# Kernel optimization log

Hardware: AMD Instinct MI355X
Metric: run time of the kernel (lower is better)

## Reference

```python
import jax, jax.numpy as jnp
import numpy as np

B, I_LEN, Q_LEN, H = 256, 256, 64, 512
MID, G, FLAT_OUT = 512, 1, 1024


def setup_inputs() -> dict:
    key = jax.random.key(0)
    ks = jax.random.split(key, 20)
    s = lambda k, sh: jax.random.normal(k, sh, dtype=jnp.float32) * 0.02
    inp = {
        'i_batch': jax.random.normal(ks[0], (B, I_LEN, H), dtype=jnp.float32),
        'q_batch': jax.random.normal(ks[1], (B, Q_LEN, H), dtype=jnp.float32),
        'i_mask': jax.random.bernoulli(ks[2], 0.1, (B, 1, 1, I_LEN)),
        'q_mask': jax.random.bernoulli(ks[3], 0.1, (B, 1, 1, Q_LEN)),
        # l_flatten (applied to i_feat) params
        'lf_w1': s(ks[4], (H, MID)), 'lf_b1': jnp.zeros((MID,), jnp.float32),
        'lf_w2': s(ks[5], (MID, G)), 'lf_b2': jnp.zeros((G,), jnp.float32),
        'lf_wm': s(ks[6], (H * G, FLAT_OUT)), 'lf_bm': jnp.zeros((FLAT_OUT,), jnp.float32),
        # i_flatten (applied to l_feat) params
        'if_w1': s(ks[7], (H, MID)), 'if_b1': jnp.zeros((MID,), jnp.float32),
        'if_w2': s(ks[8], (MID, G)), 'if_b2': jnp.zeros((G,), jnp.float32),
        'if_wm': s(ks[9], (H * G, FLAT_OUT)), 'if_bm': jnp.zeros((FLAT_OUT,), jnp.float32),
        # fh_h: Linear(1024, 512)
        'fh_w': s(ks[10], (FLAT_OUT, 512)), 'fh_b': jnp.zeros((512,), jnp.float32),
    }
    return inp


def _qkv_attention(query, key, value, mask):
    # query [B,Lq,H], key/value [B,Lk,H], mask [B,1,1,Lk] (True = pad)
    d_k = query.shape[-1]
    scores = jnp.einsum('bqh,bkh->bqk', query, key) / jnp.sqrt(jnp.asarray(d_k, query.dtype))
    scores = jnp.where(mask[:, 0], jnp.asarray(-65504.0, scores.dtype), scores)
    p_attn = jax.nn.softmax(scores, axis=-1)
    return jnp.einsum('bqk,bkh->bqh', p_attn, value)


def _att_flat(x, x_mask, w1, b1, w2, b2, wm, bm):
    # x [B,L,H], x_mask [B,1,1,L]
    att = jnp.maximum(x @ w1 + b1, 0.0) @ w2 + b2           # [B,L,G]
    att = jnp.where(x_mask[:, 0, 0, :, None], -1e9, att)
    att = jax.nn.softmax(att, axis=1)
    pooled = jnp.einsum('blg,blh->bgh', att, x).reshape(x.shape[0], -1)  # [B,G*H]
    return pooled @ wm + bm, att[..., 0]                    # att.squeeze() with G=1


def reference(i_batch, q_batch, i_mask, q_mask,
              lf_w1, lf_b1, lf_w2, lf_b2, lf_wm, lf_bm,
              if_w1, if_b1, if_w2, if_b2, if_wm, if_bm,
              fh_w, fh_b):
    i_feat = _qkv_attention(i_batch, q_batch, q_batch, q_mask)   # [B,I_LEN,H]
    i_feat, i_weight = _att_flat(i_feat, i_mask, lf_w1, lf_b1, lf_w2, lf_b2, lf_wm, lf_bm)
    l_feat = _qkv_attention(q_batch, i_batch, i_batch, i_mask)   # [B,Q_LEN,H]
    l_feat, _ = _att_flat(l_feat, q_mask, if_w1, if_b1, if_w2, if_b2, if_wm, if_bm)
    out = (l_feat + i_feat) @ fh_w + fh_b                        # [B,512]
    return out, i_weight
```

## Files before the change

kernel.cpp:

```cpp
#include <hip/hip_runtime.h>
#include <math.h>


#define SCALE 0.04419417382415922f

typedef __attribute__((ext_vector_type(8))) short short8;
typedef __attribute__((ext_vector_type(4))) float floatx4;

__device__ __forceinline__ unsigned short f2bf(float x) {
  unsigned u = __float_as_uint(x);
  unsigned r = u + 0x7FFFu + ((u >> 16) & 1u);
  return (unsigned short)(r >> 16);
}
__device__ __forceinline__ float bf2f(unsigned short h) {
  return __uint_as_float(((unsigned)h) << 16);
}
__device__ __forceinline__ unsigned pk2(float a, float b) {
  return (unsigned)f2bf(a) | ((unsigned)f2bf(b) << 16);
}

__device__ __forceinline__ float wave_max(float v) {
#pragma unroll
  for (int o = 32; o > 0; o >>= 1) v = fmaxf(v, __shfl_xor(v, o, 64));
  return v;
}
__device__ __forceinline__ float wave_sum(float v) {
#pragma unroll
  for (int o = 32; o > 0; o >>= 1) v += __shfl_xor(v, o, 64);
  return v;
}

#define GLD_LDS16(gptr, lptr)                                             \
  __builtin_amdgcn_global_load_lds(                                       \
      (const __attribute__((address_space(1))) void*)(gptr),              \
      (__attribute__((address_space(3))) void*)(lptr), 16, 0, 0)

__global__ __launch_bounds__(256) void k_prep(
    const float* __restrict__ ib, const float* __restrict__ qb,
    const float* __restrict__ lf_w1, const float* __restrict__ if_w1,
    const float* __restrict__ lf_wm, const float* __restrict__ if_wm,
    const float* __restrict__ fh_w, unsigned short* __restrict__ ib_bf,
    unsigned short* __restrict__ ibT, unsigned short* __restrict__ qb_bf,
    unsigned short* __restrict__ w1t_lf, unsigned short* __restrict__ w1t_if,
    unsigned short* __restrict__ wcat_t, unsigned short* __restrict__ fh_wt) {
  __shared__ __align__(16) char smem[64 * 65 * 4];
  const int idx = blockIdx.x, t = threadIdx.x;

  if (idx < 512) {
    float(*T)[65] = (float(*)[65])smem;
    const float* src;
    unsigned short* dst;
    int N, ds, koff, k0, n0;
    if (idx < 64) {
      src = lf_w1; dst = w1t_lf; N = 512; ds = 512; koff = 0;
      k0 = (idx & 7) * 64; n0 = (idx >> 3) * 64;
    } else if (idx < 128) {
      int l = idx - 64;
      src = if_w1; dst = w1t_if; N = 512; ds = 512; koff = 0;
      k0 = (l & 7) * 64; n0 = (l >> 3) * 64;
    } else if (idx < 256) {
      int l = idx - 128;
      src = lf_wm; dst = wcat_t; N = 1024; ds = 1024; koff = 0;
      k0 = (l & 7) * 64; n0 = (l >> 3) * 64;
    } else if (idx < 384) {
      int l = idx - 256;
      src = if_wm; dst = wcat_t; N = 1024; ds = 1024; koff = 512;
      k0 = (l & 7) * 64; n0 = (l >> 3) * 64;
    } else {
      int l = idx - 384;
      src = fh_w; dst = fh_wt; N = 512; ds = 1024; koff = 0;
      k0 = (l & 15) * 64; n0 = (l >> 4) * 64;
    }
#pragma unroll
    for (int i = 0; i < 16; i++) {
      int e = t + i * 256, r = e >> 6, c = e & 63;
      T[r][c] = src[(size_t)(k0 + r) * N + n0 + c];
    }
    __syncthreads();
#pragma unroll
    for (int i = 0; i < 8; i++) {
      int e = t + i * 256, r = e >> 5, c2 = (e & 31) * 2;
      *(unsigned*)&dst[(size_t)(n0 + r) * ds + koff + k0 + c2] =
          pk2(T[c2][r], T[c2 + 1][r]);
    }
  } else if (idx < 4608) {
    int j = idx - 512;
    int b = j >> 4, tok0 = ((j >> 2) & 3) * 64, h0 = (j & 3) * 128;
    unsigned short* Tb = (unsigned short*)smem;
    const float* src = ib + ((size_t)b * 256 + tok0) * 512 + h0;
#pragma unroll
    for (int i = 0; i < 8; i++) {
      int e = t + i * 256, tok = e >> 5, h4 = (e & 31) * 4;
      float4 v = *(const float4*)&src[(size_t)tok * 512 + h4];
      uint2 p;
      p.x = pk2(v.x, v.y);
      p.y = pk2(v.z, v.w);
      int col = ((((h4 >> 3) ^ (tok >> 3)) & 15) << 3) | (h4 & 7);
      *(uint2*)&Tb[tok * 128 + col] = p;
    }
    __syncthreads();
    unsigned short* dbf = ib_bf + ((size_t)b * 256 + tok0) * 512 + h0;
#pragma unroll
    for (int i = 0; i < 4; i++) {
      int e = t + i * 256, tok = e >> 4, g = e & 15;
      int sg = (g ^ (tok >> 3)) & 15;
      *(uint4*)&dbf[(size_t)tok * 512 + g * 8] = *(const uint4*)&Tb[tok * 128 + sg * 8];
    }
    unsigned short* dT = ibT + ((size_t)b * 512 + h0) * 256 + tok0;
#pragma unroll
    for (int i = 0; i < 4; i++) {
      int e = t + i * 256, h = e >> 3, tc = (e & 7) * 8;
      int hg = h >> 3, ho = h & 7;
      unsigned y[8];
#pragma unroll
      for (int k = 0; k < 8; k++) {
        int r = tc + k;
        y[k] = Tb[r * 128 + (((hg ^ (r >> 3)) & 15) << 3) + ho];
      }
      uint4 v;
      v.x = y[0] | (y[1] << 16);
      v.y = y[2] | (y[3] << 16);
      v.z = y[4] | (y[5] << 16);
      v.w = y[6] | (y[7] << 16);
      *(uint4*)&dT[(size_t)h * 256 + tc] = v;
    }
  } else {
    int j = idx - 4608;
    const float4* src = (const float4*)(qb + (size_t)j * 4096);
    uint2* dst = (uint2*)(qb_bf + (size_t)j * 4096);
#pragma unroll
    for (int i = 0; i < 4; i++) {
      int e = t + i * 256;
      float4 v = src[e];
      uint2 p;
      p.x = pk2(v.x, v.y);
      p.y = pk2(v.z, v.w);
      dst[e] = p;
    }
  }
}

__global__ __launch_bounds__(256) void k_scores_f(
    const unsigned short* __restrict__ ibf, const unsigned short* __restrict__ qbf,
    const int* __restrict__ imask, const int* __restrict__ qmask,
    unsigned short* __restrict__ P1, unsigned short* __restrict__ P2,
    float* __restrict__ psum) {
  __shared__ unsigned short As[64 * 64];
  __shared__ unsigned short Bs[128 * 64];
  __shared__ __align__(16) unsigned short X[128 * 72];
  const int b = blockIdx.y, ic = blockIdx.x, i0 = ic * 128;
  const int t = threadIdx.x, w = t >> 6, lane = t & 63, c = lane & 15, qq = lane >> 4;

  floatx4 acc[4][2];
#pragma unroll
  for (int ti = 0; ti < 4; ti++)
#pragma unroll
    for (int tj = 0; tj < 2; tj++) acc[ti][tj] = (floatx4){0.f, 0.f, 0.f, 0.f};

  for (int k0 = 0; k0 < 512; k0 += 64) {
#pragma unroll
    for (int i = 0; i < 2; i++) {
      int s = i * 256 + t, row = s >> 3, src = (s & 7) ^ (row & 7);
      GLD_LDS16(qbf + ((size_t)b * 64 + row) * 512 + k0 + src * 8,
                &As[(i * 256 + w * 64) * 8]);
    }
#pragma unroll
    for (int i = 0; i < 4; i++) {
      int s = i * 256 + t, row = s >> 3, src = (s & 7) ^ (row & 7);
      GLD_LDS16(ibf + ((size_t)b * 256 + i0 + row) * 512 + k0 + src * 8,
                &Bs[(i * 256 + w * 64) * 8]);
    }
    __syncthreads();
#pragma unroll
    for (int kk = 0; kk < 2; kk++) {
      short8 a[4], bb[2];
#pragma unroll
      for (int ti = 0; ti < 4; ti++)
        a[ti] = *(const short8*)&As[(ti * 16 + c) * 64 + ((kk * 4 + qq) ^ (c & 7)) * 8];
#pragma unroll
      for (int tj = 0; tj < 2; tj++)
        bb[tj] = *(const short8*)&Bs[(w * 32 + tj * 16 + c) * 64 + ((kk * 4 + qq) ^ (c & 7)) * 8];
#pragma unroll
      for (int ti = 0; ti < 4; ti++)
#pragma unroll
        for (int tj = 0; tj < 2; tj++)
          acc[ti][tj] = __builtin_amdgcn_mfma_f32_16x16x32_bf16(a[ti], bb[tj], acc[ti][tj], 0, 0, 0);
    }
    __syncthreads();
  }

  const int il0 = w * 32 + c;
  int imsk0 = imask[b * 256 + i0 + il0];
  int imsk1 = imask[b * 256 + i0 + il0 + 16];
  int qm[4][4];
#pragma unroll
  for (int ti = 0; ti < 4; ti++)
#pragma unroll
    for (int rr = 0; rr < 4; rr++) qm[ti][rr] = qmask[b * 64 + ti * 16 + qq * 4 + rr];

#pragma unroll
  for (int ti = 0; ti < 4; ti++)
#pragma unroll
    for (int rr = 0; rr < 4; rr++) {
      int qv = ti * 16 + qq * 4 + rr;
      float e0 = imsk0 ? 0.f : __expf(acc[ti][0][rr] * SCALE);
      float e1 = imsk1 ? 0.f : __expf(acc[ti][1][rr] * SCALE);
      X[qv * 136 + il0] = f2bf(e0);
      X[qv * 136 + il0 + 16] = f2bf(e1);
      float s = e0 + e1;
#pragma unroll
      for (int o = 1; o <= 8; o <<= 1) s += __shfl_xor(s, o, 64);
      if (c == 0) psum[((size_t)(b * 64 + qv)) * 8 + ic * 4 + w] = s;
    }
  __syncthreads();
#pragma unroll
  for (int i = 0; i < 4; i++) {
    int e2 = t + i * 256, qv = e2 >> 4, g = e2 & 15;
    *(uint4*)&P2[((size_t)b * 64 + qv) * 256 + i0 + g * 8] = *(const uint4*)&X[qv * 136 + g * 8];
  }
  __syncthreads();

#pragma unroll
  for (int tj = 0; tj < 2; tj++) {
    float ev[4][4];
    float s1 = 0.f;
#pragma unroll
    for (int ti = 0; ti < 4; ti++)
#pragma unroll
      for (int rr = 0; rr < 4; rr++) {
        ev[ti][rr] = qm[ti][rr] ? 0.f : __expf(acc[ti][tj][rr] * SCALE);
        s1 += ev[ti][rr];
      }
    s1 += __shfl_xor(s1, 16, 64);
    s1 += __shfl_xor(s1, 32, 64);
    float inv = 1.f / s1;
    int il = il0 + tj * 16;
#pragma unroll
    for (int ti = 0; ti < 4; ti++)
#pragma unroll
      for (int rr = 0; rr < 4; rr++)
        X[il * 72 + ti * 16 + qq * 4 + rr] = f2bf(ev[ti][rr] * inv);
  }
  __syncthreads();
#pragma unroll
  for (int i = 0; i < 4; i++) {
    int e2 = t + i * 256, il = e2 >> 3, g = e2 & 7;
    *(uint4*)&P1[((size_t)b * 256 + i0 + il) * 64 + g * 8] = *(const uint4*)&X[il * 72 + g * 8];
  }
}

__global__ __launch_bounds__(256) void k_av2(const unsigned short* __restrict__ P2,
                                             const unsigned short* __restrict__ ibT,
                                             const float* __restrict__ psum,
                                             unsigned short* __restrict__ lfeat) {
  __shared__ unsigned short As[64 * 64];
  __shared__ unsigned short Bs[128 * 64];
  const int b = blockIdx.y, n0 = blockIdx.x * 128;
  const int t = threadIdx.x, w = t >> 6, lane = t & 63, c = lane & 15, q = lane >> 4;
  const int wm = w >> 1, wn = w & 1;
  floatx4 acc[2][4];
#pragma unroll
  for (int ti = 0; ti < 2; ti++)
#pragma unroll
    for (int tj = 0; tj < 4; tj++) acc[ti][tj] = (floatx4){0.f, 0.f, 0.f, 0.f};

  for (int kc = 0; kc < 256; kc += 64) {
#pragma unroll
    for (int i = 0; i < 2; i++) {
      int s = i * 256 + t, row = s >> 3, src = (s & 7) ^ (row & 7);
      GLD_LDS16(P2 + ((size_t)b * 64 + row) * 256 + kc + src * 8, &As[(i * 256 + w * 64) * 8]);
    }
#pragma unroll
    for (int i = 0; i < 4; i++) {
      int s = i * 256 + t, row = s >> 3, src = (s & 7) ^ (row & 7);
      GLD_LDS16(ibT + ((size_t)b * 512 + n0 + row) * 256 + kc + src * 8,
                &Bs[(i * 256 + w * 64) * 8]);
    }
    __syncthreads();
#pragma unroll
    for (int kk = 0; kk < 2; kk++) {
      short8 a[2], bb[4];
#pragma unroll
      for (int ti = 0; ti < 2; ti++)
        a[ti] = *(const short8*)&As[(wm * 32 + ti * 16 + c) * 64 + ((kk * 4 + q) ^ (c & 7)) * 8];
#pragma unroll
      for (int tj = 0; tj < 4; tj++)
        bb[tj] = *(const short8*)&Bs[(wn * 64 + tj * 16 + c) * 64 + ((kk * 4 + q) ^ (c & 7)) * 8];
#pragma unroll
      for (int ti = 0; ti < 2; ti++)
#pragma unroll
        for (int tj = 0; tj < 4; tj++)
          acc[ti][tj] = __builtin_amdgcn_mfma_f32_16x16x32_bf16(a[ti], bb[tj], acc[ti][tj], 0, 0, 0);
    }
    __syncthreads();
  }
#pragma unroll
  for (int ti = 0; ti < 2; ti++)
#pragma unroll
    for (int rr = 0; rr < 4; rr++) {
      int m = wm * 32 + ti * 16 + q * 4 + rr;
      const float* ps = psum + ((size_t)(b * 64 + m)) * 8;
      float s = ps[0] + ps[1] + ps[2] + ps[3] + ps[4] + ps[5] + ps[6] + ps[7];
      float inv = 1.f / s;
      unsigned short* op = lfeat + ((size_t)b * 64 + m) * 512 + n0 + wn * 64;
#pragma unroll
      for (int tj = 0; tj < 4; tj++) op[tj * 16 + c] = f2bf(acc[ti][tj][rr] * inv);
    }
}

__global__ __launch_bounds__(256) void k_qbw1(const unsigned short* __restrict__ qbf,
                                              const unsigned short* __restrict__ W1t,
                                              unsigned short* __restrict__ qbW1T) {
  __shared__ unsigned short As[64 * 64];
  __shared__ unsigned short Bs[128 * 64];
  const int b = blockIdx.y, n0 = blockIdx.x * 128;
  const int t = threadIdx.x, w = t >> 6, lane = t & 63, c = lane & 15, q = lane >> 4;
  const int wm = w >> 1, wn = w & 1;
  floatx4 acc[2][4];
#pragma unroll
  for (int ti = 0; ti < 2; ti++)
#pragma unroll
    for (int tj = 0; tj < 4; tj++) acc[ti][tj] = (floatx4){0.f, 0.f, 0.f, 0.f};

  for (int k0 = 0; k0 < 512; k0 += 64) {
#pragma unroll
    for (int i = 0; i < 2; i++) {
      int s = i * 256 + t, row = s >> 3, src = (s & 7) ^ (row & 7);
      GLD_LDS16(qbf + ((size_t)b * 64 + row) * 512 + k0 + src * 8,
                &As[(i * 256 + w * 64) * 8]);
    }
#pragma unroll
    for (int i = 0; i < 4; i++) {
      int s = i * 256 + t, row = s >> 3, src = (s & 7) ^ (row & 7);
      GLD_LDS16(W1t + (size_t)(n0 + row) * 512 + k0 + src * 8,
                &Bs[(i * 256 + w * 64) * 8]);
    }
    __syncthreads();
#pragma unroll
    for (int kk = 0; kk < 2; kk++) {
      short8 a[2], bb[4];
#pragma unroll
      for (int ti = 0; ti < 2; ti++)
        a[ti] = *(const short8*)&As[(wm * 32 + ti * 16 + c) * 64 + ((kk * 4 + q) ^ (c & 7)) * 8];
#pragma unroll
      for (int tj = 0; tj < 4; tj++)
        bb[tj] = *(const short8*)&Bs[(wn * 64 + tj * 16 + c) * 64 + ((kk * 4 + q) ^ (c & 7)) * 8];
#pragma unroll
      for (int ti = 0; ti < 2; ti++)
#pragma unroll
        for (int tj = 0; tj < 4; tj++)
          acc[ti][tj] = __builtin_amdgcn_mfma_f32_16x16x32_bf16(a[ti], bb[tj], acc[ti][tj], 0, 0, 0);
    }
    __syncthreads();
  }
#pragma unroll
  for (int ti = 0; ti < 2; ti++)
#pragma unroll
    for (int tj = 0; tj < 4; tj++) {
      int n = n0 + wn * 64 + tj * 16 + c;
      int m = wm * 32 + ti * 16 + q * 4;
      uint2 p;
      p.x = pk2(acc[ti][tj][0], acc[ti][tj][1]);
      p.y = pk2(acc[ti][tj][2], acc[ti][tj][3]);
      *(uint2*)&qbW1T[((size_t)b * 512 + n) * 64 + m] = p;
    }
}

__global__ __launch_bounds__(256) void k_logits_i64(
    const unsigned short* __restrict__ P1, const unsigned short* __restrict__ qbW1T,
    const float* __restrict__ b1, const float* __restrict__ w2,
    float* __restrict__ outp) {
  __shared__ unsigned short As[128 * 64];
  __shared__ unsigned short Bs[128 * 64];
  __shared__ float red[2][128];
  const int b = blockIdx.y;
  const int mt = blockIdx.x & 1, nc = blockIdx.x >> 1;
  const int m0 = mt * 128, n0 = nc * 128;
  const int t = threadIdx.x, w = t >> 6, lane = t & 63, c = lane & 15, q = lane >> 4;
  const int wm = w >> 1, wn = w & 1;

#pragma unroll
  for (int i = 0; i < 4; i++) {
    int s = i * 256 + t, row = s >> 3, src = (s & 7) ^ (row & 7);
    GLD_LDS16(P1 + ((size_t)b * 256 + m0 + row) * 64 + src * 8, &As[(i * 256 + w * 64) * 8]);
  }
#pragma unroll
  for (int i = 0; i < 4; i++) {
    int s = i * 256 + t, row = s >> 3, src = (s & 7) ^ (row & 7);
    GLD_LDS16(qbW1T + ((size_t)b * 512 + n0 + row) * 64 + src * 8, &Bs[(i * 256 + w * 64) * 8]);
  }
  __syncthreads();
  floatx4 acc[4][4];
#pragma unroll
  for (int ti = 0; ti < 4; ti++)
#pragma unroll
    for (int tj = 0; tj < 4; tj++) acc[ti][tj] = (floatx4){0.f, 0.f, 0.f, 0.f};
#pragma unroll
  for (int kk = 0; kk < 2; kk++) {
    short8 a[4], bb[4];
#pragma unroll
    for (int ti = 0; ti < 4; ti++)
      a[ti] = *(const short8*)&As[(wm * 64 + ti * 16 + c) * 64 + ((kk * 4 + q) ^ (c & 7)) * 8];
#pragma unroll
    for (int tj = 0; tj < 4; tj++)
      bb[tj] = *(const short8*)&Bs[(wn * 64 + tj * 16 + c) * 64 + ((kk * 4 + q) ^ (c & 7)) * 8];
#pragma unroll
    for (int ti = 0; ti < 4; ti++)
#pragma unroll
      for (int tj = 0; tj < 4; tj++)
        acc[ti][tj] = __builtin_amdgcn_mfma_f32_16x16x32_bf16(a[ti], bb[tj], acc[ti][tj], 0, 0, 0);
  }

  float partial[4][4] = {};
#pragma unroll
  for (int tj = 0; tj < 4; tj++) {
    int n = n0 + wn * 64 + tj * 16 + c;
    float bia = b1[n], wwv = w2[n];
#pragma unroll
    for (int ti = 0; ti < 4; ti++)
#pragma unroll
      for (int r = 0; r < 4; r++)
        partial[ti][r] += fmaxf(acc[ti][tj][r] + bia, 0.f) * wwv;
  }
#pragma unroll
  for (int msk = 1; msk <= 8; msk <<= 1)
#pragma unroll
    for (int ti = 0; ti < 4; ti++)
#pragma unroll
      for (int r = 0; r < 4; r++)
        partial[ti][r] += __shfl_xor(partial[ti][r], msk, 64);
  if (c == 0) {
#pragma unroll
    for (int ti = 0; ti < 4; ti++)
#pragma unroll
      for (int r = 0; r < 4; r++)
        red[wn][wm * 64 + ti * 16 + q * 4 + r] = partial[ti][r];
  }
  __syncthreads();
  if (t < 128) outp[(size_t)nc * 65536 + b * 256 + m0 + t] = red[0][t] + red[1][t];
}

__global__ __launch_bounds__(256) void k_logits_part(
    const unsigned short* __restrict__ X, const unsigned short* __restrict__ W1t,
    const float* __restrict__ b1, const float* __restrict__ w2,
    float* __restrict__ outp, int M) {
  __shared__ unsigned short As[128 * 64];
  __shared__ unsigned short Bs[128 * 64];
  __shared__ float red[2][128];
  const int t = threadIdx.x, w = t >> 6, lane = t & 63;
  const int wm = w >> 1, wn = w & 1, c = lane & 15, q = lane >> 4;
  const int idx = blockIdx.x;
  const int m_tile = (idx & 7) + ((idx >> 5) << 3), nc = (idx >> 3) & 3;
  const int m0 = m_tile * 128, n0 = nc * 128;

  floatx4 acc[4][4];
#pragma unroll
  for (int ti = 0; ti < 4; ti++)
#pragma unroll
    for (int tj = 0; tj < 4; tj++) acc[ti][tj] = (floatx4){0.f, 0.f, 0.f, 0.f};

  for (int k0 = 0; k0 < 512; k0 += 64) {
#pragma unroll
    for (int it = 0; it < 4; it++) {
      int s = it * 256 + t, row = s >> 3, src = (s & 7) ^ (row & 7);
      GLD_LDS16(X + (size_t)(m0 + row) * 512 + k0 + src * 8, &As[(it * 256 + w * 64) * 8]);
      GLD_LDS16(W1t + (size_t)(n0 + row) * 512 + k0 + src * 8, &Bs[(it * 256 + w * 64) * 8]);
    }
    __syncthreads();
#pragma unroll
    for (int kk = 0; kk < 2; kk++) {
      short8 a[4], bb[4];
#pragma unroll
      for (int ti = 0; ti < 4; ti++)
        a[ti] = *(const short8*)&As[(wm * 64 + ti * 16 + c) * 64 + ((kk * 4 + q) ^ (c & 7)) * 8];
#pragma unroll
      for (int tj = 0; tj < 4; tj++)
        bb[tj] = *(const short8*)&Bs[(wn * 64 + tj * 16 + c) * 64 + ((kk * 4 + q) ^ (c & 7)) * 8];
#pragma unroll
      for (int ti = 0; ti < 4; ti++)
#pragma unroll
        for (int tj = 0; tj < 4; tj++)
          acc[ti][tj] = __builtin_amdgcn_mfma_f32_16x16x32_bf16(a[ti], bb[tj], acc[ti][tj], 0, 0, 0);
    }
    __syncthreads();
  }
  float partial[4][4] = {};
#pragma unroll
  for (int tj = 0; tj < 4; tj++) {
    int n = n0 + wn * 64 + tj * 16 + c;
    float bia = b1[n], wwv = w2[n];
#pragma unroll
    for (int ti = 0; ti < 4; ti++)
#pragma unroll
      for (int r = 0; r < 4; r++)
        partial[ti][r] += fmaxf(acc[ti][tj][r] + bia, 0.f) * wwv;
  }
#pragma unroll
  for (int msk = 1; msk <= 8; msk <<= 1)
#pragma unroll
    for (int ti = 0; ti < 4; ti++)
#pragma unroll
      for (int r = 0; r < 4; r++)
        partial[ti][r] += __shfl_xor(partial[ti][r], msk, 64);
  if (c == 0) {
#pragma unroll
    for (int ti = 0; ti < 4; ti++)
#pragma unroll
      for (int r = 0; r < 4; r++)
        red[wn][wm * 64 + ti * 16 + q * 4 + r] = partial[ti][r];
  }
  __syncthreads();
  if (t < 128) outp[(size_t)nc * M + m0 + t] = red[0][t] + red[1][t];
}

__global__ __launch_bounds__(256) void k_attsoft_i(const float* __restrict__ lp,
                                                   const int* __restrict__ imask,
                                                   float* __restrict__ att,
                                                   float* __restrict__ iw_out) {
  __shared__ float red[4];
  const int b = blockIdx.x, t = threadIdx.x;
  const int i = b * 256 + t;
  float x = lp[i] + lp[65536 + i] + lp[131072 + i] + lp[196608 + i];
  float v = imask[i] ? -1e9f : x;
  float wm = wave_max(v);
  if ((t & 63) == 0) red[t >> 6] = wm;
  __syncthreads();
  float mx = fmaxf(fmaxf(red[0], red[1]), fmaxf(red[2], red[3]));
  __syncthreads();
  float e = __expf(v - mx);
  float wsum = wave_sum(e);
  if ((t & 63) == 0) red[t >> 6] = wsum;
  __syncthreads();
  float s = red[0] + red[1] + red[2] + red[3];
  float p = e / s;
  att[i] = p;
  iw_out[i] = p;
}

__global__ __launch_bounds__(64) void k_attsoft_l(const float* __restrict__ lp,
                                                  const int* __restrict__ qmask,
                                                  float* __restrict__ att) {
  const int b = blockIdx.x, t = threadIdx.x;
  const int i = b * 64 + t;
  float x = lp[i] + lp[16384 + i] + lp[32768 + i] + lp[49152 + i];
  float v = qmask[i] ? -1e9f : x;
  float mx = wave_max(v);
  float e = __expf(v - mx);
  float s = wave_sum(e);
  att[i] = e / s;
}

__global__ __launch_bounds__(256) void k_attp(const float* __restrict__ att,
                                              const unsigned short* __restrict__ P1,
                                              float* __restrict__ v) {
  __shared__ float av[256];
  __shared__ float red[4][64];
  const int b = blockIdx.x, t = threadIdx.x;
  const int part = t >> 6, lane = t & 63;
  av[t] = att[b * 256 + t];
  __syncthreads();
  const unsigned short* Pb = P1 + ((size_t)b * 256 + part * 64) * 64 + lane;
  float s0 = 0.f, s1 = 0.f;
#pragma unroll 8
  for (int ii = 0; ii < 64; ii += 2) {
    s0 += av[part * 64 + ii] * bf2f(Pb[(size_t)ii * 64]);
    s1 += av[part * 64 + ii + 1] * bf2f(Pb[(size_t)(ii + 1) * 64]);
  }
  red[part][lane] = s0 + s1;
  __syncthreads();
  if (t < 64) v[b * 64 + t] = red[0][t] + red[1][t] + red[2][t] + red[3][t];
}

__global__ __launch_bounds__(256) void k_pooled(const unsigned short* __restrict__ X,
                                                const float* __restrict__ att, int L,
                                                unsigned short* __restrict__ out,
                                                int ooff) {
  __shared__ float ar[256];
  const int b = blockIdx.x, t = threadIdx.x;
  if (t < L) ar[t] = att[b * L + t];
  __syncthreads();
  float a0 = 0.f, a1 = 0.f;
  const unsigned short* Xb = X + (size_t)b * L * 512 + 2 * t;
#pragma unroll 4
  for (int l = 0; l < L; l++) {
    unsigned u = *(const unsigned*)&Xb[(size_t)l * 512];
    float a = ar[l];
    a0 += a * bf2f((unsigned short)(u & 0xffff));
    a1 += a * bf2f((unsigned short)(u >> 16));
  }
  *(unsigned*)&out[(size_t)b * 1024 + ooff + 2 * t] = pk2(a0, a1);
}

__global__ __launch_bounds__(256) void k_egemm(const unsigned short* __restrict__ X,
                                               const unsigned short* __restrict__ Wt,
                                               const float* __restrict__ biasA,
                                               const float* __restrict__ biasB,
                                               float* __restrict__ outf,
                                               unsigned short* __restrict__ outbf,
                                               int N, int K) {
  __shared__ unsigned short As[64 * 64];
  __shared__ unsigned short Bs[64 * 64];
  const int n0 = blockIdx.x * 64, m0 = blockIdx.y * 64;
  const int t = threadIdx.x, w = t >> 6, lane = t & 63, c = lane & 15, q = lane >> 4;
  const int wm = w >> 1, wn = w & 1;
  floatx4 acc[2][2];
#pragma unroll
  for (int ti = 0; ti < 2; ti++)
#pragma unroll
    for (int tj = 0; tj < 2; tj++) acc[ti][tj] = (floatx4){0.f, 0.f, 0.f, 0.f};

  for (int k0 = 0; k0 < K; k0 += 64) {
#pragma unroll
    for (int i = 0; i < 2; i++) {
      int s = i * 256 + t, row = s >> 3, src = (s & 7) ^ (row & 7);
      GLD_LDS16(X + (size_t)(m0 + row) * K + k0 + src * 8, &As[(i * 256 + w * 64) * 8]);
      GLD_LDS16(Wt + (size_t)(n0 + row) * K + k0 + src * 8, &Bs[(i * 256 + w * 64) * 8]);
    }
    __syncthreads();
#pragma unroll
    for (int kk = 0; kk < 2; kk++) {
      short8 a[2], bb[2];
#pragma unroll
      for (int ti = 0; ti < 2; ti++)
        a[ti] = *(const short8*)&As[(wm * 32 + ti * 16 + c) * 64 + ((kk * 4 + q) ^ (c & 7)) * 8];
#pragma unroll
      for (int tj = 0; tj < 2; tj++)
        bb[tj] = *(const short8*)&Bs[(wn * 32 + tj * 16 + c) * 64 + ((kk * 4 + q) ^ (c & 7)) * 8];
#pragma unroll
      for (int ti = 0; ti < 2; ti++)
#pragma unroll
        for (int tj = 0; tj < 2; tj++)
          acc[ti][tj] = __builtin_amdgcn_mfma_f32_16x16x32_bf16(a[ti], bb[tj], acc[ti][tj], 0, 0, 0);
    }
    __syncthreads();
  }
#pragma unroll
  for (int tj = 0; tj < 2; tj++) {
    int n = n0 + wn * 32 + tj * 16 + c;
    float bias = biasA[n] + (biasB ? biasB[n] : 0.f);
#pragma unroll
    for (int ti = 0; ti < 2; ti++)
#pragma unroll
      for (int rr = 0; rr < 4; rr++) {
        int m = m0 + wm * 32 + ti * 16 + q * 4 + rr;
        float v = acc[ti][tj][rr] + bias;
        if (outbf) outbf[(size_t)m * N + n] = f2bf(v);
        else outf[(size_t)m * N + n] = v;
      }
  }
}

extern "C" void kernel_launch(void* const* d_in, const int* in_sizes, int n_in,
                              void* d_out, int out_size, void* d_ws, size_t ws_size,
                              hipStream_t stream) {
  const float* ib = (const float*)d_in[0];
  const float* qb = (const float*)d_in[1];
  const int* imask = (const int*)d_in[2];
  const int* qmask = (const int*)d_in[3];
  const float* lf_w1 = (const float*)d_in[4];
  const float* lf_b1 = (const float*)d_in[5];
  const float* lf_w2 = (const float*)d_in[6];
  const float* lf_wm = (const float*)d_in[8];
  const float* lf_bm = (const float*)d_in[9];
  const float* if_w1 = (const float*)d_in[10];
  const float* if_b1 = (const float*)d_in[11];
  const float* if_w2 = (const float*)d_in[12];
  const float* if_wm = (const float*)d_in[14];
  const float* if_bm = (const float*)d_in[15];
  const float* fh_w = (const float*)d_in[16];
  const float* fh_b = (const float*)d_in[17];
  float* out = (float*)d_out;

  float* lp_i = (float*)d_ws;
  float* lp_l = lp_i + 262144;
  float* att_i = lp_l + 65536;
  float* att_l = att_i + 65536;
  float* psum = att_l + 16384;
  unsigned short* P1 = (unsigned short*)(psum + 131072);
  unsigned short* P2 = P1 + 4194304;
  unsigned short* ib_bf = P2 + 4194304;
  unsigned short* qb_bf = ib_bf + 33554432;
  unsigned short* qbW1T = qb_bf + 8388608;
  unsigned short* ibT = qbW1T + 8388608;
  unsigned short* w1t_lf = ibT + 33554432;
  unsigned short* w1t_if = w1t_lf + 262144;
  unsigned short* wcat_t = w1t_if + 262144;
  unsigned short* fh_wt = wcat_t + 1048576;
  unsigned short* pooled_bf = fh_wt + 524288;
  unsigned short* F_bf = pooled_bf + 262144;
  unsigned short* lfeat = ib_bf;
  float* v_i = psum;

  k_prep<<<6656, 256, 0, stream>>>(ib, qb, lf_w1, if_w1, lf_wm, if_wm, fh_w,
                                   ib_bf, ibT, qb_bf, w1t_lf, w1t_if,
                                   wcat_t, fh_wt);

  k_scores_f<<<dim3(2, 256), 256, 0, stream>>>(ib_bf, qb_bf, imask, qmask, P1, P2, psum);
  k_av2<<<dim3(4, 256), 256, 0, stream>>>(P2, ibT, psum, lfeat);
  k_qbw1<<<dim3(4, 256), 256, 0, stream>>>(qb_bf, w1t_lf, qbW1T);
  k_logits_i64<<<dim3(8, 256), 256, 0, stream>>>(P1, qbW1T, lf_b1, lf_w2, lp_i);
  k_logits_part<<<512, 256, 0, stream>>>(lfeat, w1t_if, if_b1, if_w2, lp_l, 16384);
  k_attsoft_i<<<256, 256, 0, stream>>>(lp_i, imask, att_i, out + 131072);
  k_attsoft_l<<<256, 64, 0, stream>>>(lp_l, qmask, att_l);
  k_attp<<<256, 256, 0, stream>>>(att_i, P1, v_i);
  k_pooled<<<256, 256, 0, stream>>>(qb_bf, v_i, 64, pooled_bf, 0);
  k_pooled<<<256, 256, 0, stream>>>(lfeat, att_l, 64, pooled_bf, 512);

  k_egemm<<<dim3(16, 4), 256, 0, stream>>>(pooled_bf, wcat_t, lf_bm, if_bm,
                                           nullptr, F_bf, 1024, 1024);
  k_egemm<<<dim3(8, 4), 256, 0, stream>>>(F_bf, fh_wt, fh_b, nullptr,
                                          out, nullptr, 512, 1024);
}
```

Baseline: 416.9 us.

## Convert i_batch to bf16 inside scores kernel and fuse tail softmax/pooling kernels

The prep kernel no longer writes a row-major bf16 copy of i_batch. Instead k_scores_f reads fp32 i_batch directly and converts it to bf16 while staging into swizzled LDS, which removes a 64MB write and a later read. The five small tail kernels (two softmaxes, attention-P reduction, two pooling passes) are merged into two fused kernels, removing launches and intermediate buffers. In exchange the scores kernel reads twice as many bytes through ordinary register loads rather than async global-to-LDS loads, so that copy no longer overlaps with the rest of the kernel.

Measured after the change: 416.2 us. No clear change (-0.2%).

```diff
diff --git a/kernel.cpp b/kernel.cpp
--- a/kernel.cpp
+++ b/kernel.cpp
@@ -39,10 +39,10 @@
     const float* __restrict__ ib, const float* __restrict__ qb,
     const float* __restrict__ lf_w1, const float* __restrict__ if_w1,
     const float* __restrict__ lf_wm, const float* __restrict__ if_wm,
-    const float* __restrict__ fh_w, unsigned short* __restrict__ ib_bf,
-    unsigned short* __restrict__ ibT, unsigned short* __restrict__ qb_bf,
-    unsigned short* __restrict__ w1t_lf, unsigned short* __restrict__ w1t_if,
-    unsigned short* __restrict__ wcat_t, unsigned short* __restrict__ fh_wt) {
+    const float* __restrict__ fh_w, unsigned short* __restrict__ ibT,
+    unsigned short* __restrict__ qb_bf, unsigned short* __restrict__ w1t_lf,
+    unsigned short* __restrict__ w1t_if, unsigned short* __restrict__ wcat_t,
+    unsigned short* __restrict__ fh_wt) {
   __shared__ __align__(16) char smem[64 * 65 * 4];
   const int idx = blockIdx.x, t = threadIdx.x;
 
@@ -99,13 +99,6 @@
       *(uint2*)&Tb[tok * 128 + col] = p;
     }
     __syncthreads();
-    unsigned short* dbf = ib_bf + ((size_t)b * 256 + tok0) * 512 + h0;
-#pragma unroll
-    for (int i = 0; i < 4; i++) {
-      int e = t + i * 256, tok = e >> 4, g = e & 15;
-      int sg = (g ^ (tok >> 3)) & 15;
-      *(uint4*)&dbf[(size_t)tok * 512 + g * 8] = *(const uint4*)&Tb[tok * 128 + sg * 8];
-    }
     unsigned short* dT = ibT + ((size_t)b * 512 + h0) * 256 + tok0;
 #pragma unroll
     for (int i = 0; i < 4; i++) {
@@ -141,7 +134,7 @@
 }
 
 __global__ __launch_bounds__(256) void k_scores_f(
-    const unsigned short* __restrict__ ibf, const unsigned short* __restrict__ qbf,
+    const float* __restrict__ ib, const unsigned short* __restrict__ qbf,
     const int* __restrict__ imask, const int* __restrict__ qmask,
     unsigned short* __restrict__ P1, unsigned short* __restrict__ P2,
     float* __restrict__ psum) {
@@ -165,10 +158,14 @@
                 &As[(i * 256 + w * 64) * 8]);
     }
 #pragma unroll
-    for (int i = 0; i < 4; i++) {
-      int s = i * 256 + t, row = s >> 3, src = (s & 7) ^ (row & 7);
-      GLD_LDS16(ibf + ((size_t)b * 256 + i0 + row) * 512 + k0 + src * 8,
-                &Bs[(i * 256 + w * 64) * 8]);
+    for (int i = 0; i < 8; i++) {
+      int s = i * 256 + t, row = s >> 4, c4 = s & 15;
+      float4 v = *(const float4*)&ib[((size_t)b * 256 + i0 + row) * 512 + k0 + c4 * 4];
+      int gs = (c4 >> 1) ^ (row & 7), sub = c4 & 1;
+      uint2 p;
+      p.x = pk2(v.x, v.y);
+      p.y = pk2(v.z, v.w);
+      *(uint2*)&Bs[row * 64 + gs * 8 + sub * 4] = p;
     }
     __syncthreads();
 #pragma unroll
@@ -513,82 +510,84 @@
   if (t < 128) outp[(size_t)nc * M + m0 + t] = red[0][t] + red[1][t];
 }
 
-__global__ __launch_bounds__(256) void k_attsoft_i(const float* __restrict__ lp,
-                                                   const int* __restrict__ imask,
-                                                   float* __restrict__ att,
-                                                   float* __restrict__ iw_out) {
-  __shared__ float red[4];
+__global__ __launch_bounds__(256) void k_final_i(const float* __restrict__ lp,
+                                                 const int* __restrict__ imask,
+                                                 const unsigned short* __restrict__ P1,
+                                                 const unsigned short* __restrict__ qbf,
+                                                 float* __restrict__ iw_out,
+                                                 unsigned short* __restrict__ pooled) {
+  __shared__ float red4[4];
+  __shared__ float ar[256];
+  __shared__ float red[4][64];
+  __shared__ float vsm[64];
   const int b = blockIdx.x, t = threadIdx.x;
   const int i = b * 256 + t;
   float x = lp[i] + lp[65536 + i] + lp[131072 + i] + lp[196608 + i];
   float v = imask[i] ? -1e9f : x;
-  float wm = wave_max(v);
-  if ((t & 63) == 0) red[t >> 6] = wm;
-  __syncthreads();
-  float mx = fmaxf(fmaxf(red[0], red[1]), fmaxf(red[2], red[3]));
+  float wmx = wave_max(v);
+  if ((t & 63) == 0) red4[t >> 6] = wmx;
+  __syncthreads();
+  float mx = fmaxf(fmaxf(red4[0], red4[1]), fmaxf(red4[2], red4[3]));
   __syncthreads();
   float e = __expf(v - mx);
-  float wsum = wave_sum(e);
-  if ((t & 63) == 0) red[t >> 6] = wsum;
-  __syncthreads();
-  float s = red[0] + red[1] + red[2] + red[3];
+  float ws = wave_sum(e);
+  if ((t & 63) == 0) red4[t >> 6] = ws;
+  __syncthreads();
+  float s = red4[0] + red4[1] + red4[2] + red4[3];
   float p = e / s;
-  att[i] = p;
   iw_out[i] = p;
-}
-
-__global__ __launch_bounds__(64) void k_attsoft_l(const float* __restrict__ lp,
-                                                  const int* __restrict__ qmask,
-                                                  float* __restrict__ att) {
-  const int b = blockIdx.x, t = threadIdx.x;
-  const int i = b * 64 + t;
-  float x = lp[i] + lp[16384 + i] + lp[32768 + i] + lp[49152 + i];
-  float v = qmask[i] ? -1e9f : x;
-  float mx = wave_max(v);
-  float e = __expf(v - mx);
-  float s = wave_sum(e);
-  att[i] = e / s;
-}
-
-__global__ __launch_bounds__(256) void k_attp(const float* __restrict__ att,
-                                              const unsigned short* __restrict__ P1,
-                                              float* __restrict__ v) {
-  __shared__ float av[256];
-  __shared__ float red[4][64];
-  const int b = blockIdx.x, t = threadIdx.x;
+  ar[t] = p;
+  __syncthreads();
   const int part = t >> 6, lane = t & 63;
-  av[t] = att[b * 256 + t];
-  __syncthreads();
   const unsigned short* Pb = P1 + ((size_t)b * 256 + part * 64) * 64 + lane;
   float s0 = 0.f, s1 = 0.f;
 #pragma unroll 8
   for (int ii = 0; ii < 64; ii += 2) {
-    s0 += av[part * 64 + ii] * bf2f(Pb[(size_t)ii * 64]);
-    s1 += av[part * 64 + ii + 1] * bf2f(Pb[(size_t)(ii + 1) * 64]);
+    s0 += ar[part * 64 + ii] * bf2f(Pb[(size_t)ii * 64]);
+    s1 += ar[part * 64 + ii + 1] * bf2f(Pb[(size_t)(ii + 1) * 64]);
   }
   red[part][lane] = s0 + s1;
   __syncthreads();
-  if (t < 64) v[b * 64 + t] = red[0][t] + red[1][t] + red[2][t] + red[3][t];
-}
-
-__global__ __launch_bounds__(256) void k_pooled(const unsigned short* __restrict__ X,
-                                                const float* __restrict__ att, int L,
-                                                unsigned short* __restrict__ out,
-                                                int ooff) {
-  __shared__ float ar[256];
+  if (t < 64) vsm[t] = red[0][t] + red[1][t] + red[2][t] + red[3][t];
+  __syncthreads();
+  float a0 = 0.f, a1 = 0.f;
+  const unsigned short* Xb = qbf + (size_t)b * 64 * 512 + 2 * t;
+#pragma unroll 4
+  for (int l = 0; l < 64; l++) {
+    unsigned u = *(const unsigned*)&Xb[(size_t)l * 512];
+    float a = vsm[l];
+    a0 += a * bf2f((unsigned short)(u & 0xffff));
+    a1 += a * bf2f((unsigned short)(u >> 16));
+  }
+  *(unsigned*)&pooled[(size_t)b * 1024 + 2 * t] = pk2(a0, a1);
+}
+
+__global__ __launch_bounds__(256) void k_final_l(const float* __restrict__ lp,
+                                                 const int* __restrict__ qmask,
+                                                 const unsigned short* __restrict__ lfeat,
+                                                 unsigned short* __restrict__ pooled) {
+  __shared__ float ar[64];
   const int b = blockIdx.x, t = threadIdx.x;
-  if (t < L) ar[t] = att[b * L + t];
+  if (t < 64) {
+    const int i = b * 64 + t;
+    float x = lp[i] + lp[16384 + i] + lp[32768 + i] + lp[49152 + i];
+    float v = qmask[i] ? -1e9f : x;
+    float mx = wave_max(v);
+    float e = __expf(v - mx);
+    float s = wave_sum(e);
+    ar[t] = e / s;
+  }
   __syncthreads();
   float a0 = 0.f, a1 = 0.f;
-  const unsigned short* Xb = X + (size_t)b * L * 512 + 2 * t;
+  const unsigned short* Xb = lfeat + (size_t)b * 64 * 512 + 2 * t;
 #pragma unroll 4
-  for (int l = 0; l < L; l++) {
+  for (int l = 0; l < 64; l++) {
     unsigned u = *(const unsigned*)&Xb[(size_t)l * 512];
     float a = ar[l];
     a0 += a * bf2f((unsigned short)(u & 0xffff));
     a1 += a * bf2f((unsigned short)(u >> 16));
   }
-  *(unsigned*)&out[(size_t)b * 1024 + ooff + 2 * t] = pk2(a0, a1);
+  *(unsigned*)&pooled[(size_t)b * 1024 + 512 + 2 * t] = pk2(a0, a1);
 }
 
 __global__ __launch_bounds__(256) void k_egemm(const unsigned short* __restrict__ X,
@@ -678,8 +677,8 @@
   float* psum = att_l + 16384;
   unsigned short* P1 = (unsigned short*)(psum + 131072);
   unsigned short* P2 = P1 + 4194304;
-  unsigned short* ib_bf = P2 + 4194304;
-  unsigned short* qb_bf = ib_bf + 33554432;
+  unsigned short* lfeat = P2 + 4194304;
+  unsigned short* qb_bf = lfeat + 33554432;
   unsigned short* qbW1T = qb_bf + 8388608;
   unsigned short* ibT = qbW1T + 8388608;
   unsigned short* w1t_lf = ibT + 33554432;
@@ -688,23 +687,17 @@
   unsigned short* fh_wt = wcat_t + 1048576;
   unsigned short* pooled_bf = fh_wt + 524288;
   unsigned short* F_bf = pooled_bf + 262144;
-  unsigned short* lfeat = ib_bf;
-  float* v_i = psum;
 
   k_prep<<<6656, 256, 0, stream>>>(ib, qb, lf_w1, if_w1, lf_wm, if_wm, fh_w,
-                                   ib_bf, ibT, qb_bf, w1t_lf, w1t_if,
-                                   wcat_t, fh_wt);
-
-  k_scores_f<<<dim3(2, 256), 256, 0, stream>>>(ib_bf, qb_bf, imask, qmask, P1, P2, psum);
+                                   ibT, qb_bf, w1t_lf, w1t_if, wcat_t, fh_wt);
+
+  k_scores_f<<<dim3(2, 256), 256, 0, stream>>>(ib, qb_bf, imask, qmask, P1, P2, psum);
   k_av2<<<dim3(4, 256), 256, 0, stream>>>(P2, ibT, psum, lfeat);
   k_qbw1<<<dim3(4, 256), 256, 0, stream>>>(qb_bf, w1t_lf, qbW1T);
   k_logits_i64<<<dim3(8, 256), 256, 0, stream>>>(P1, qbW1T, lf_b1, lf_w2, lp_i);
   k_logits_part<<<512, 256, 0, stream>>>(lfeat, w1t_if, if_b1, if_w2, lp_l, 16384);
-  k_attsoft_i<<<256, 256, 0, stream>>>(lp_i, imask, att_i, out + 131072);
-  k_attsoft_l<<<256, 64, 0, stream>>>(lp_l, qmask, att_l);
-  k_attp<<<256, 256, 0, stream>>>(att_i, P1, v_i);
-  k_pooled<<<256, 256, 0, stream>>>(qb_bf, v_i, 64, pooled_bf, 0);
-  k_pooled<<<256, 256, 0, stream>>>(lfeat, att_l, 64, pooled_bf, 512);
+  k_final_i<<<256, 256, 0, stream>>>(lp_i, imask, P1, qb_bf, out + 131072, pooled_bf);
+  k_final_l<<<256, 256, 0, stream>>>(lp_l, qmask, lfeat, pooled_bf);
 
   k_egemm<<<dim3(16, 4), 256, 0, stream>>>(pooled_bf, wcat_t, lf_bm, if_bm,
                                            nullptr, F_bf, 1024, 1024);
```
